# Kernel optimization log

Hardware: AMD Instinct MI355X
Metric: run time of the kernel (lower is better)

The kernel has to match this reference:

```python
import jax, jax.numpy as jnp
import numpy as np
import math

NUM_HEADS = 32
NUM_KV_HEADS = 8
HEAD_DIM = 64
ROPE_THETA = 150000.0


def rotate_half(x):
    half = x.shape[-1] // 2
    return jnp.concatenate([-x[..., half:], x[..., :half]], axis=-1)


def setup_inputs() -> dict:
    key = jax.random.key(0)
    k1, k2, k3, k4, k5 = jax.random.split(key, 5)
    B, S, H = 2, 2048, 2048
    qkv_size = (NUM_HEADS + 2 * NUM_KV_HEADS) * HEAD_DIM  # 3072
    scale = 1.0 / math.sqrt(H)
    return {
        "hidden_states": jax.random.normal(k1, (B, S, H), jnp.float32),
        "position_ids": jnp.arange(S, dtype=jnp.int64 if jax.config.jax_enable_x64 else jnp.int32)[None, :],
        "qkv_w": jax.random.normal(k2, (qkv_size, H), jnp.float32) * scale,
        "qkv_b": jax.random.normal(k3, (qkv_size,), jnp.float32) * 0.01,
        "o_w": jax.random.normal(k4, (H, NUM_HEADS * HEAD_DIM), jnp.float32) * scale,
        "o_b": jax.random.normal(k5, (H,), jnp.float32) * 0.01,
    }


def reference(hidden_states, position_ids, qkv_w, qkv_b, o_w, o_b):
    B, S, _ = hidden_states.shape
    g = NUM_HEADS // NUM_KV_HEADS  # query heads per kv head
    d = HEAD_DIM

    qkv = hidden_states @ qkv_w.T + qkv_b  # [B,S,(H+2KV)*d]
    qkv = qkv.reshape(B, S, NUM_KV_HEADS, g + 2, d)
    q = qkv[:, :, :, :g, :].reshape(B, S, NUM_HEADS, d).transpose(0, 2, 1, 3)   # [B,Hq,S,d]
    k = qkv[:, :, :, g, :].transpose(0, 2, 1, 3)                                 # [B,Hkv,S,d]
    v = qkv[:, :, :, g + 1, :].transpose(0, 2, 1, 3)                             # [B,Hkv,S,d]

    # HF-style RoPE: cos/sin [S, d]
    inv_freq = 1.0 / (ROPE_THETA ** (jnp.arange(0, d, 2, dtype=jnp.float32) / d))
    freqs = jnp.outer(position_ids.reshape(-1).astype(jnp.float32), inv_freq)    # [S, d/2]
    emb = jnp.concatenate([freqs, freqs], axis=-1)                               # [S, d]
    cos = jnp.cos(emb)[None, None]                                               # [1,1,S,d]
    sin = jnp.sin(emb)[None, None]
    q = q * cos + rotate_half(q) * sin
    k = k * cos + rotate_half(k) * sin

    # GQA: repeat_interleave kv heads to match query heads
    k = jnp.repeat(k, g, axis=1)  # [B,Hq,S,d]
    v = jnp.repeat(v, g, axis=1)

    scores = jnp.einsum("bhqd,bhkd->bhqk", q, k) / math.sqrt(d)  # [B,Hq,S,S]
    attn = jax.nn.softmax(scores, axis=-1)
    out = jnp.einsum("bhqk,bhkd->bhqd", attn, v)
    out = out.transpose(0, 2, 1, 3).reshape(B, S, NUM_HEADS * d)
    return out @ o_w.T + o_b
```

## Files before the change

### kernel.cpp

```cpp
#include <hip/hip_runtime.h>
#include <math.h>

#define NHQ 32
#define NKV 8
#define HD 64
#define QKV_DIM 3072
#define MODEL_DIM 2048
#define QSCALE 0.1803368801111204f

typedef __attribute__((ext_vector_type(4))) float     f32x4;
typedef __attribute__((ext_vector_type(8))) _Float16  half8;
typedef __attribute__((ext_vector_type(4))) _Float16  half4v;
typedef __attribute__((ext_vector_type(2))) __fp16    fp16x2;

#define ASYNC_COPY16(g, l)                                                        \
    __builtin_amdgcn_global_load_lds(                                             \
        (const __attribute__((address_space(1))) void*)(g),                       \
        (__attribute__((address_space(3))) void*)(l), 16, 0, 0)

__device__ __forceinline__ float fast_exp2(float x)
{
#if __has_builtin(__builtin_amdgcn_exp2f)
    return __builtin_amdgcn_exp2f(x);
#else
    float r;
    asm volatile("v_exp_f32 %0, %1\ns_nop 0" : "=v"(r) : "v"(x));
    return r;
#endif
}

__global__ __launch_bounds__(256)
void f32_to_f16_kernel(const float* __restrict__ src, _Float16* __restrict__ dst, int n4)
{
    int i = blockIdx.x * 256 + threadIdx.x;
    if (i < n4) {
        float4 v = ((const float4*)src)[i];
        half4v h = { (_Float16)v.x, (_Float16)v.y, (_Float16)v.z, (_Float16)v.w };
        ((half4v*)dst)[i] = h;
    }
}

__global__ __launch_bounds__(256)
void sincos_table_kernel(const int* __restrict__ pos, float* __restrict__ tab, int S)
{
    int i = blockIdx.x * 256 + threadIdx.x;
    if (i < S * 32) {
        int s = i >> 5, fi = i & 31;
        float p = (float)pos[s];
        float inv_freq = powf(150000.0f, -(float)fi * (1.0f / 32.0f));
        float ang = p * inv_freq;
        tab[s * 64 + fi]      = cosf(ang);
        tab[s * 64 + 32 + fi] = sinf(ang);
    }
}

template<int MODE>
__global__ __launch_bounds__(256)
void gemm_f16_mfma(const _Float16* __restrict__ A, const _Float16* __restrict__ W,
                   const float* __restrict__ bias, void* __restrict__ Cout,
                   const float* __restrict__ tab, int M, int N, int K, int S)
{
    __shared__ _Float16 As[128 * 32];
    __shared__ _Float16 Bs[128 * 32];

    const int t    = threadIdx.x;
    const int w    = t >> 6;
    const int lane = t & 63;
    const int quad = lane >> 4, l15 = lane & 15;
    const size_t m0 = (size_t)blockIdx.y * 128;
    const size_t n0 = (size_t)blockIdx.x * 128;
    const int wm = (w >> 1) * 64, wn = (w & 1) * 64;

    const int row0 = t >> 2;
    const int sub  = (t & 3) * 8;
    const _Float16* ag0 = A + (m0 + row0) * K + sub;
    const _Float16* ag1 = A + (m0 + 64 + row0) * K + sub;
    const _Float16* bg0 = W + (n0 + row0) * K + sub;
    const _Float16* bg1 = W + (n0 + 64 + row0) * K + sub;
    _Float16* al0 = &As[w * 512];
    _Float16* al1 = &As[2048 + w * 512];
    _Float16* bl0 = &Bs[w * 512];
    _Float16* bl1 = &Bs[2048 + w * 512];

    f32x4 acc[4][4];
#pragma unroll
    for (int i = 0; i < 4; i++)
#pragma unroll
        for (int j = 0; j < 4; j++) acc[i][j] = (f32x4){0.f, 0.f, 0.f, 0.f};

    for (int k0 = 0; k0 < K; k0 += 32) {
        ASYNC_COPY16(ag0 + k0, al0);
        ASYNC_COPY16(ag1 + k0, al1);
        ASYNC_COPY16(bg0 + k0, bl0);
        ASYNC_COPY16(bg1 + k0, bl1);
        __syncthreads();

        half8 af[4], bf[4];
#pragma unroll
        for (int i = 0; i < 4; i++) {
            af[i] = *(const half8*)&As[(wm + i * 16 + l15) * 32 + quad * 8];
            bf[i] = *(const half8*)&Bs[(wn + i * 16 + l15) * 32 + quad * 8];
        }
#pragma unroll
        for (int i = 0; i < 4; i++)
#pragma unroll
            for (int j = 0; j < 4; j++)
                acc[i][j] = __builtin_amdgcn_mfma_f32_16x16x32_f16(af[i], bf[j], acc[i][j], 0, 0, 0);
        __syncthreads();
    }

    float bv[4];
#pragma unroll
    for (int j = 0; j < 4; j++) bv[j] = bias[n0 + wn + j * 16 + l15];

    const int ct = (int)(((n0 + wn) >> 6) % 6);

#pragma unroll
    for (int i = 0; i < 4; i++)
#pragma unroll
        for (int r = 0; r < 4; r++) {
            const size_t row = m0 + wm + i * 16 + quad * 4 + r;
            float v[4];
#pragma unroll
            for (int j = 0; j < 4; j++) v[j] = acc[i][j][r] + bv[j];

            if (MODE == 2 && ct != 5) {
                const float* tc = tab + (size_t)(row % S) * 64;
                const float ca = tc[l15],      sa = tc[32 + l15];
                const float cb = tc[16 + l15], sb = tc[48 + l15];
                const float qs = (ct < 4) ? QSCALE : 1.0f;
                const float n0v = v[0] * ca - v[2] * sa;
                const float n1v = v[1] * cb - v[3] * sb;
                const float n2v = v[2] * ca + v[0] * sa;
                const float n3v = v[3] * cb + v[1] * sb;
                v[0] = n0v * qs; v[1] = n1v * qs; v[2] = n2v * qs; v[3] = n3v * qs;
            }

            const size_t col = n0 + wn + l15;
#pragma unroll
            for (int j = 0; j < 4; j++) {
                if (MODE != 0) ((_Float16*)Cout)[row * N + col + j * 16] = (_Float16)v[j];
                else           ((float*)Cout)[row * N + col + j * 16] = v[j];
            }
        }
}

__global__ __launch_bounds__(256)
void transpose_v_kernel(const _Float16* __restrict__ qkv, _Float16* __restrict__ vtg, int BS)
{
    __shared__ _Float16 tile[64 * 72];
    const int t = threadIdx.x;
    const int tb = blockIdx.x * 64;
    const int g = blockIdx.y;
    const int voff = (g * 6 + 5) * 64;

    const int tok = t >> 2, dsub = (t & 3) * 16;
    const _Float16* src = qkv + (size_t)(tb + tok) * QKV_DIM + voff + dsub;
    *(half8*)&tile[tok * 72 + dsub]     = *(const half8*)(src);
    *(half8*)&tile[tok * 72 + dsub + 8] = *(const half8*)(src + 8);
    __syncthreads();

    const int d = t >> 2, tsub = (t & 3) * 16;
    half8 a, c;
#pragma unroll
    for (int i = 0; i < 8; i++) a[i] = tile[(tsub + i) * 72 + d];
#pragma unroll
    for (int i = 0; i < 8; i++) c[i] = tile[(tsub + 8 + i) * 72 + d];
    _Float16* dst = vtg + ((size_t)g * 64 + d) * BS + tb + tsub;
    *(half8*)dst       = a;
    *(half8*)(dst + 8) = c;
}

__global__ __launch_bounds__(256)
void attn_mfma(const _Float16* __restrict__ qkv, const _Float16* __restrict__ vtg,
               _Float16* __restrict__ out, int B, int S)
{
    __shared__ _Float16 Ks[64 * 72];
    __shared__ _Float16 VsT[80 * 72];
    __shared__ _Float16 Ps[4][32 * 72];

    const int t = threadIdx.x, w = t >> 6, lane = t & 63;
    const int quad = lane >> 4, l15 = lane & 15;
    const int b = blockIdx.z, g = blockIdx.y;
    const int q0 = blockIdx.x * 32;
    const int qoff = (g * 6 + w) * 64;
    const int koff = (g * 6 + 4) * 64;

    half8 qf[2][2];
#pragma unroll
    for (int s = 0; s < 2; s++) {
        const _Float16* qp = qkv + (size_t)(b * S + q0 + s * 16 + l15) * QKV_DIM + qoff;
        qf[s][0] = *(const half8*)(qp + quad * 8);
        qf[s][1] = *(const half8*)(qp + 32 + quad * 8);
    }

    for (int idx = 64 * 72 + t; idx < 80 * 72; idx += 256)
        VsT[idx] = (idx < 65 * 72) ? (_Float16)1.0f : (_Float16)0.0f;

    f32x4 O[2][4], L[2];
#pragma unroll
    for (int s = 0; s < 2; s++) {
        L[s] = (f32x4){0.f, 0.f, 0.f, 0.f};
#pragma unroll
        for (int dt = 0; dt < 4; dt++) O[s][dt] = (f32x4){0.f, 0.f, 0.f, 0.f};
    }

    const int kst_tok = t >> 2;
    const int kst_d   = (t & 3) * 16;
    const int vst_d   = t >> 3;
    const int vst_sub = (t & 7) * 8;

    const _Float16* kbase  = qkv + (size_t)(b * S + kst_tok) * QKV_DIM + koff + kst_d;
    const _Float16* vbase0 = vtg + ((size_t)g * 64 + vst_d) * (size_t)(B * S) + b * S + vst_sub;
    const _Float16* vbase1 = vtg + ((size_t)g * 64 + 32 + vst_d) * (size_t)(B * S) + b * S + vst_sub;

    half8 kr0 = *(const half8*)(kbase);
    half8 kr1 = *(const half8*)(kbase + 8);
    half8 vr0 = *(const half8*)(vbase0);
    half8 vr1 = *(const half8*)(vbase1);

    for (int kt = 0; kt < S; kt += 64) {
        *(half8*)&Ks[kst_tok * 72 + kst_d]      = kr0;
        *(half8*)&Ks[kst_tok * 72 + kst_d + 8]  = kr1;
        *(half8*)&VsT[vst_d * 72 + vst_sub]        = vr0;
        *(half8*)&VsT[(32 + vst_d) * 72 + vst_sub] = vr1;
        __syncthreads();

        if (kt + 64 < S) {
            kr0 = *(const half8*)(kbase + (size_t)(kt + 64) * QKV_DIM);
            kr1 = *(const half8*)(kbase + (size_t)(kt + 64) * QKV_DIM + 8);
            vr0 = *(const half8*)(vbase0 + kt + 64);
            vr1 = *(const half8*)(vbase1 + kt + 64);
        }

        half8 kf[4][2];
#pragma unroll
        for (int mt = 0; mt < 4; mt++) {
            kf[mt][0] = *(const half8*)&Ks[(mt * 16 + l15) * 72 + quad * 8];
            kf[mt][1] = *(const half8*)&Ks[(mt * 16 + l15) * 72 + 32 + quad * 8];
        }
        f32x4 sacc[2][4];
#pragma unroll
        for (int s = 0; s < 2; s++)
#pragma unroll
            for (int mt = 0; mt < 4; mt++) {
                f32x4 z = (f32x4){0.f, 0.f, 0.f, 0.f};
                z = __builtin_amdgcn_mfma_f32_16x16x32_f16(kf[mt][0], qf[s][0], z, 0, 0, 0);
                z = __builtin_amdgcn_mfma_f32_16x16x32_f16(kf[mt][1], qf[s][1], z, 0, 0, 0);
                sacc[s][mt] = z;
            }

#pragma unroll
        for (int s = 0; s < 2; s++)
#pragma unroll
            for (int mt = 0; mt < 4; mt++) {
                fp16x2 pa = __builtin_amdgcn_cvt_pkrtz(fast_exp2(sacc[s][mt][0]),
                                                       fast_exp2(sacc[s][mt][1]));
                fp16x2 pb = __builtin_amdgcn_cvt_pkrtz(fast_exp2(sacc[s][mt][2]),
                                                       fast_exp2(sacc[s][mt][3]));
                uint2 u;
                u.x = __builtin_bit_cast(unsigned int, pa);
                u.y = __builtin_bit_cast(unsigned int, pb);
                *(uint2*)&Ps[w][(s * 16 + l15) * 72 + mt * 16 + quad * 4] = u;
            }
        asm volatile("s_waitcnt lgkmcnt(0)" ::: "memory");

        half8 pf[2][2];
#pragma unroll
        for (int s = 0; s < 2; s++) {
            pf[s][0] = *(const half8*)&Ps[w][(s * 16 + l15) * 72 + quad * 8];
            pf[s][1] = *(const half8*)&Ps[w][(s * 16 + l15) * 72 + 32 + quad * 8];
        }
#pragma unroll
        for (int dt = 0; dt < 4; dt++) {
            half8 vv0 = *(const half8*)&VsT[(dt * 16 + l15) * 72 + quad * 8];
            half8 vv1 = *(const half8*)&VsT[(dt * 16 + l15) * 72 + 32 + quad * 8];
#pragma unroll
            for (int s = 0; s < 2; s++) {
                O[s][dt] = __builtin_amdgcn_mfma_f32_16x16x32_f16(pf[s][0], vv0, O[s][dt], 0, 0, 0);
                O[s][dt] = __builtin_amdgcn_mfma_f32_16x16x32_f16(pf[s][1], vv1, O[s][dt], 0, 0, 0);
            }
        }
        {
            half8 lv0 = *(const half8*)&VsT[(64 + l15) * 72 + quad * 8];
            half8 lv1 = *(const half8*)&VsT[(64 + l15) * 72 + 32 + quad * 8];
#pragma unroll
            for (int s = 0; s < 2; s++) {
                L[s] = __builtin_amdgcn_mfma_f32_16x16x32_f16(pf[s][0], lv0, L[s], 0, 0, 0);
                L[s] = __builtin_amdgcn_mfma_f32_16x16x32_f16(pf[s][1], lv1, L[s], 0, 0, 0);
            }
        }
        __syncthreads();
    }

    const int hq = g * 4 + w;
#pragma unroll
    for (int s = 0; s < 2; s++)
#pragma unroll
        for (int r = 0; r < 4; r++) {
            const float lr = __shfl(L[s][r], lane & 48, 64);
            const float ir = 1.0f / lr;
            const size_t row = (size_t)(b * S + q0 + s * 16 + quad * 4 + r);
#pragma unroll
            for (int dt = 0; dt < 4; dt++)
                out[row * (NHQ * HD) + hq * 64 + dt * 16 + l15] = (_Float16)(O[s][dt][r] * ir);
        }
}

extern "C" void kernel_launch(void* const* d_in, const int* in_sizes, int n_in,
                              void* d_out, int out_size, void* d_ws, size_t ws_size,
                              hipStream_t stream)
{
    const float* hidden = (const float*)d_in[0];
    const int*   pos    = (const int*)d_in[1];
    const float* qkv_w  = (const float*)d_in[2];
    const float* qkv_b  = (const float*)d_in[3];
    const float* o_w    = (const float*)d_in[4];
    const float* o_b    = (const float*)d_in[5];
    float* out = (float*)d_out;

    const int S  = in_sizes[1];
    const int BS = in_sizes[0] / MODEL_DIM;
    const int B  = BS / S;

    _Float16* hA   = (_Float16*)d_ws;
    _Float16* hW1  = hA   + (size_t)BS * MODEL_DIM;
    _Float16* hW2  = hW1  + (size_t)QKV_DIM * MODEL_DIM;
    _Float16* qkvh = hW2  + (size_t)MODEL_DIM * MODEL_DIM;
    _Float16* atth = qkvh + (size_t)BS * QKV_DIM;
    float*    tab  = (float*)(atth + (size_t)BS * MODEL_DIM);
    _Float16* vtg  = (_Float16*)(tab + (size_t)S * 64);

    f32_to_f16_kernel<<<(BS * MODEL_DIM / 4 + 255) / 256, 256, 0, stream>>>(hidden, hA, BS * MODEL_DIM / 4);
    f32_to_f16_kernel<<<(QKV_DIM * MODEL_DIM / 4 + 255) / 256, 256, 0, stream>>>(qkv_w, hW1, QKV_DIM * MODEL_DIM / 4);
    f32_to_f16_kernel<<<(MODEL_DIM * MODEL_DIM / 4 + 255) / 256, 256, 0, stream>>>(o_w, hW2, MODEL_DIM * MODEL_DIM / 4);
    sincos_table_kernel<<<(S * 32 + 255) / 256, 256, 0, stream>>>(pos, tab, S);

    gemm_f16_mfma<2><<<dim3(QKV_DIM / 128, BS / 128), 256, 0, stream>>>(
        hA, hW1, qkv_b, qkvh, tab, BS, QKV_DIM, MODEL_DIM, S);

    transpose_v_kernel<<<dim3(BS / 64, NKV), 256, 0, stream>>>(qkvh, vtg, BS);

    attn_mfma<<<dim3(S / 32, NKV, B), 256, 0, stream>>>(qkvh, vtg, atth, B, S);

    gemm_f16_mfma<0><<<dim3(MODEL_DIM / 128, BS / 128), 256, 0, stream>>>(
        atth, hW2, o_b, out, nullptr, BS, MODEL_DIM, MODEL_DIM, S);
}
```

Measured before the change: 345.0 us.

## Merge setup kernels into one launch and alias K tile with P buffers

Measured after the change: 350.2 us. Within noise of the previous version (+1.5%).

```diff
diff --git a/kernel.cpp b/kernel.cpp
--- a/kernel.cpp
+++ b/kernel.cpp
@@ -30,27 +30,31 @@
 }
 
 __global__ __launch_bounds__(256)
-void f32_to_f16_kernel(const float* __restrict__ src, _Float16* __restrict__ dst, int n4)
+void setup_kernel(const float* __restrict__ ha, const float* __restrict__ hb,
+                  const float* __restrict__ hc, _Float16* __restrict__ da,
+                  _Float16* __restrict__ db, _Float16* __restrict__ dc,
+                  const int* __restrict__ pos, float* __restrict__ tab,
+                  int n4a, int n4b, int n4c, int S)
 {
     int i = blockIdx.x * 256 + threadIdx.x;
-    if (i < n4) {
-        float4 v = ((const float4*)src)[i];
+    if (i < n4a + n4b + n4c) {
+        const float* src; _Float16* dst; int j;
+        if (i < n4a)            { src = ha; dst = da; j = i; }
+        else if (i < n4a + n4b) { src = hb; dst = db; j = i - n4a; }
+        else                    { src = hc; dst = dc; j = i - n4a - n4b; }
+        float4 v = ((const float4*)src)[j];
         half4v h = { (_Float16)v.x, (_Float16)v.y, (_Float16)v.z, (_Float16)v.w };
-        ((half4v*)dst)[i] = h;
-    }
-}
-
-__global__ __launch_bounds__(256)
-void sincos_table_kernel(const int* __restrict__ pos, float* __restrict__ tab, int S)
-{
-    int i = blockIdx.x * 256 + threadIdx.x;
-    if (i < S * 32) {
-        int s = i >> 5, fi = i & 31;
-        float p = (float)pos[s];
-        float inv_freq = powf(150000.0f, -(float)fi * (1.0f / 32.0f));
-        float ang = p * inv_freq;
-        tab[s * 64 + fi]      = cosf(ang);
-        tab[s * 64 + 32 + fi] = sinf(ang);
+        ((half4v*)dst)[j] = h;
+    } else {
+        int k = i - (n4a + n4b + n4c);
+        if (k < S * 32) {
+            int s = k >> 5, fi = k & 31;
+            float p = (float)pos[s];
+            float inv_freq = powf(150000.0f, -(float)fi * (1.0f / 32.0f));
+            float ang = p * inv_freq;
+            tab[s * 64 + fi]      = cosf(ang);
+            tab[s * 64 + 32 + fi] = sinf(ang);
+        }
     }
 }
 
@@ -175,9 +179,8 @@
 void attn_mfma(const _Float16* __restrict__ qkv, const _Float16* __restrict__ vtg,
                _Float16* __restrict__ out, int B, int S)
 {
-    __shared__ _Float16 Ks[64 * 72];
+    __shared__ _Float16 KP[4 * 32 * 72];
     __shared__ _Float16 VsT[80 * 72];
-    __shared__ _Float16 Ps[4][32 * 72];
 
     const int t = threadIdx.x, w = t >> 6, lane = t & 63;
     const int quad = lane >> 4, l15 = lane & 15;
@@ -186,6 +189,8 @@
     const int qoff = (g * 6 + w) * 64;
     const int koff = (g * 6 + 4) * 64;
 
+    _Float16* Ps = &KP[w * 2304];
+
     half8 qf[2][2];
 #pragma unroll
     for (int s = 0; s < 2; s++) {
@@ -220,8 +225,8 @@
     half8 vr1 = *(const half8*)(vbase1);
 
     for (int kt = 0; kt < S; kt += 64) {
-        *(half8*)&Ks[kst_tok * 72 + kst_d]      = kr0;
-        *(half8*)&Ks[kst_tok * 72 + kst_d + 8]  = kr1;
+        *(half8*)&KP[kst_tok * 72 + kst_d]      = kr0;
+        *(half8*)&KP[kst_tok * 72 + kst_d + 8]  = kr1;
         *(half8*)&VsT[vst_d * 72 + vst_sub]        = vr0;
         *(half8*)&VsT[(32 + vst_d) * 72 + vst_sub] = vr1;
         __syncthreads();
@@ -236,8 +241,8 @@
         half8 kf[4][2];
 #pragma unroll
         for (int mt = 0; mt < 4; mt++) {
-            kf[mt][0] = *(const half8*)&Ks[(mt * 16 + l15) * 72 + quad * 8];
-            kf[mt][1] = *(const half8*)&Ks[(mt * 16 + l15) * 72 + 32 + quad * 8];
+            kf[mt][0] = *(const half8*)&KP[(mt * 16 + l15) * 72 + quad * 8];
+            kf[mt][1] = *(const half8*)&KP[(mt * 16 + l15) * 72 + 32 + quad * 8];
         }
         f32x4 sacc[2][4];
 #pragma unroll
@@ -249,6 +254,7 @@
                 z = __builtin_amdgcn_mfma_f32_16x16x32_f16(kf[mt][1], qf[s][1], z, 0, 0, 0);
                 sacc[s][mt] = z;
             }
+        __syncthreads();
 
 #pragma unroll
         for (int s = 0; s < 2; s++)
@@ -261,15 +267,15 @@
                 uint2 u;
                 u.x = __builtin_bit_cast(unsigned int, pa);
                 u.y = __builtin_bit_cast(unsigned int, pb);
-                *(uint2*)&Ps[w][(s * 16 + l15) * 72 + mt * 16 + quad * 4] = u;
+                *(uint2*)&Ps[(s * 16 + l15) * 72 + mt * 16 + quad * 4] = u;
             }
         asm volatile("s_waitcnt lgkmcnt(0)" ::: "memory");
 
         half8 pf[2][2];
 #pragma unroll
         for (int s = 0; s < 2; s++) {
-            pf[s][0] = *(const half8*)&Ps[w][(s * 16 + l15) * 72 + quad * 8];
-            pf[s][1] = *(const half8*)&Ps[w][(s * 16 + l15) * 72 + 32 + quad * 8];
+            pf[s][0] = *(const half8*)&Ps[(s * 16 + l15) * 72 + quad * 8];
+            pf[s][1] = *(const half8*)&Ps[(s * 16 + l15) * 72 + 32 + quad * 8];
         }
 #pragma unroll
         for (int dt = 0; dt < 4; dt++) {
@@ -331,10 +337,13 @@
     float*    tab  = (float*)(atth + (size_t)BS * MODEL_DIM);
     _Float16* vtg  = (_Float16*)(tab + (size_t)S * 64);
 
-    f32_to_f16_kernel<<<(BS * MODEL_DIM / 4 + 255) / 256, 256, 0, stream>>>(hidden, hA, BS * MODEL_DIM / 4);
-    f32_to_f16_kernel<<<(QKV_DIM * MODEL_DIM / 4 + 255) / 256, 256, 0, stream>>>(qkv_w, hW1, QKV_DIM * MODEL_DIM / 4);
-    f32_to_f16_kernel<<<(MODEL_DIM * MODEL_DIM / 4 + 255) / 256, 256, 0, stream>>>(o_w, hW2, MODEL_DIM * MODEL_DIM / 4);
-    sincos_table_kernel<<<(S * 32 + 255) / 256, 256, 0, stream>>>(pos, tab, S);
+    const int n4a = BS * MODEL_DIM / 4;
+    const int n4b = QKV_DIM * MODEL_DIM / 4;
+    const int n4c = MODEL_DIM * MODEL_DIM / 4;
+    const int setup_items = n4a + n4b + n4c + S * 32;
+
+    setup_kernel<<<(setup_items + 255) / 256, 256, 0, stream>>>(
+        hidden, qkv_w, o_w, hA, hW1, hW2, pos, tab, n4a, n4b, n4c, S);
 
     gemm_f16_mfma<2><<<dim3(QKV_DIM / 128, BS / 128), 256, 0, stream>>>(
         hA, hW1, qkv_b, qkvh, tab, BS, QKV_DIM, MODEL_DIM, S);
```
